# Kernel tuning notes

Hardware: AMD Instinct MI355X
Metric: run time of the kernel (lower is better)

Reference implementation:

```python
import jax, jax.numpy as jnp
import numpy as np

B, N, H, DH, E, D_IN = 2, 2048, 8, 32, 65536, 256
O = H * DH
SCALE = float(np.sqrt(DH))


def setup_inputs() -> dict:
    key = jax.random.key(0)
    ks = jax.random.split(key, 8)
    rng = np.random.default_rng(0)
    x = jax.random.normal(ks[0], (B, N, D_IN), jnp.float32)
    adj = jax.random.uniform(ks[1], (B, N, N), jnp.float32)
    # unique edges per graph so scatter-add matches torch advanced-index +=
    flat = np.stack([rng.choice(N * N, size=E, replace=False) for _ in range(B)])
    edge_index = jnp.asarray(np.stack([flat // N, flat % N], axis=1), jnp.int32)  # [B,2,E]
    edge_attr = jax.random.normal(ks[2], (B, E, H), jnp.float32)
    mask = jnp.ones((B, N), dtype=bool)
    qkv_w = jax.random.normal(ks[3], (D_IN, 3 * O), jnp.float32) / np.sqrt(D_IN)
    qkv_b = jnp.zeros((3 * O,), jnp.float32)
    e_w1 = jax.random.normal(ks[4], (H, H), jnp.float32) / np.sqrt(H)
    e_b1 = jnp.zeros((H,), jnp.float32)
    e_w2 = jax.random.normal(ks[5], (H, H), jnp.float32) / np.sqrt(H)
    e_b2 = jnp.zeros((H,), jnp.float32)
    shifts = jnp.asarray(np.linspace(0.1, 0.8, H), jnp.float32).reshape(1, H, 1, 1)
    widths = jnp.full((1, H, 1, 1), 0.5, jnp.float32)
    self_loop_W = jnp.asarray(1.0 / DH + rng.uniform(0, 1, H), jnp.float32).reshape(1, H, 1, 1)
    return dict(x=x, adj=adj, edge_attr=edge_attr, qkv_w=qkv_w, qkv_b=qkv_b,
                e_w1=e_w1, e_b1=e_b1, e_w2=e_w2, e_b2=e_b2,
                shifts=shifts, widths=widths, self_loop_W=self_loop_W,
                edge_index=edge_index, mask=mask)


def reference(x, adj, edge_attr, qkv_w, qkv_b, e_w1, e_b1, e_w2, e_b2,
              shifts, widths, self_loop_W, edge_index, mask):
    Bq, Nq = x.shape[0], x.shape[1]
    # qkv projection -> [3,B,H,N,DH]
    qkv = (x @ qkv_w + qkv_b).reshape(Bq, Nq, 3, H, DH)
    qkv = jnp.transpose(qkv, (2, 0, 3, 1, 4))
    Q, K, V = qkv[0], qkv[1], qkv[2]
    # edge FFN applied twice (eval mode: noise/dropout are identity)
    def ffn(e):
        return jax.nn.relu(e @ e_w1 + e_b1) @ e_w2 + e_b2
    ea = ffn(ffn(edge_attr))                      # [B,E,H]
    ea = jnp.transpose(ea, (0, 2, 1))             # [B,H,E]
    # scores + learned moire adjacency bias
    scores = jnp.einsum('bhqd,bhkd->bhqk', Q, K) / SCALE
    moire = jnp.exp(-((adj[:, None] - shifts) ** 2) / (2.0 * widths ** 2))  # gaussian focus
    moire = jnp.clip(moire, 1e-6, None)
    s = scores + jnp.log(moire)                   # [B,H,N,N]
    # scatter edge features into score matrix
    u = edge_index[:, 0, :]                        # [B,E]
    v = edge_index[:, 1, :]
    bi = jnp.arange(Bq)[:, None, None]
    hi = jnp.arange(H)[None, :, None]
    s = s.at[bi, hi, u[:, None, :], v[:, None, :]].add(ea)
    # self-loop diagonal bias (non-trainable)
    s = s + jnp.eye(Nq, dtype=s.dtype)[None, None] * self_loop_W
    # mask and softmax
    m2 = mask[:, None, :] & mask[:, :, None]       # [B,N,N]
    s = jnp.where(m2[:, None], s, jnp.asarray(-1e6, s.dtype))
    attn = jax.nn.softmax(s, axis=-1)
    out = jnp.einsum('bhqk,bhkd->bhqd', attn, V)
    return jnp.transpose(out, (0, 2, 1, 3)).reshape(Bq, Nq, O)
```

## Files before the change

### kernel.cpp

```cpp
#include <hip/hip_runtime.h>

#define B_ 2
#define N_ 2048
#define H_ 8
#define DH_ 32
#define E_ 65536
#define DIN_ 256
#define KT 256
#define ECAP 32
#define QSCALE 0.2550348872f
#define LOG2E 1.4426950408889634f
#define LOG2MIN -19.931568569324174f

typedef short bf16x8 __attribute__((ext_vector_type(8)));
typedef float floatx4 __attribute__((ext_vector_type(4)));

__device__ __forceinline__ unsigned short f2b(float f){
  union { float f; unsigned int u; } v; v.f = f;
  return (unsigned short)((v.u + 0x7fffu + ((v.u >> 16) & 1u)) >> 16);
}
__device__ __forceinline__ bf16x8 f8_to_bf(const float* p){
  float4 a = *(const float4*)p, b = *(const float4*)(p + 4);
  bf16x8 r;
  r[0] = (short)f2b(a.x); r[1] = (short)f2b(a.y); r[2] = (short)f2b(a.z); r[3] = (short)f2b(a.w);
  r[4] = (short)f2b(b.x); r[5] = (short)f2b(b.y); r[6] = (short)f2b(b.z); r[7] = (short)f2b(b.w);
  return r;
}
__device__ __forceinline__ unsigned int cvt_pk_bf16(float lo, float hi){
  unsigned int r;
  asm("v_cvt_pk_bf16_f32 %0, %1, %2" : "=v"(r) : "v"(lo), "v"(hi));
  return r;
}

__global__ __launch_bounds__(256) void prep_kernel(
    const float* __restrict__ eattr,
    const float* __restrict__ w1, const float* __restrict__ b1,
    const float* __restrict__ w2, const float* __restrict__ b2,
    float* __restrict__ ea,
    const int* __restrict__ ei, int* __restrict__ cnt, unsigned int* __restrict__ pck,
    const float* __restrict__ w, unsigned short* __restrict__ wT)
{
  int bb = blockIdx.x, tid = threadIdx.x;
  if (bb < 512){
    __shared__ float W1[64], W2[64], Bv1[8], Bv2[8];
    if (tid < 64){ W1[tid] = w1[tid]; W2[tid] = w2[tid]; }
    if (tid < 8){ Bv1[tid] = b1[tid]; Bv2[tid] = b2[tid]; }
    __syncthreads();
    int gid = bb * 256 + tid;
    const float* ep = eattr + (size_t)gid * 8;
    float cur[8];
#pragma unroll
    for (int i = 0; i < 8; ++i) cur[i] = ep[i];
#pragma unroll
    for (int pass = 0; pass < 2; ++pass){
      float t[8];
#pragma unroll
      for (int j = 0; j < 8; ++j){
        float s = Bv1[j];
#pragma unroll
        for (int i = 0; i < 8; ++i) s += cur[i] * W1[i * 8 + j];
        t[j] = fmaxf(s, 0.f);
      }
#pragma unroll
      for (int j = 0; j < 8; ++j){
        float s = Bv2[j];
#pragma unroll
        for (int i = 0; i < 8; ++i) s += t[i] * W2[i * 8 + j];
        cur[j] = s;
      }
    }
    float* op = ea + (size_t)gid * 8;
#pragma unroll
    for (int j = 0; j < 8; ++j) op[j] = cur[j] * LOG2E;
  } else if (bb < 1024){
    int gid = (bb - 512) * 256 + tid;
    int b = gid >> 16, e = gid & (E_ - 1);
    int u = ei[(size_t)b * 2 * E_ + e];
    int v = ei[(size_t)b * 2 * E_ + E_ + e];
    int bucket = ((b << 11) + u) * 8 + (v >> 8);
    int slot = atomicAdd(&cnt[bucket], 1);
    if (slot < ECAP) pck[(size_t)bucket * ECAP + slot] = ((unsigned int)e << 11) | (unsigned int)v;
  } else {
    int k = bb - 1024;
    for (int c = tid; c < 768; c += 256)
      wT[(size_t)c * 256 + k] = f2b(w[(size_t)k * 768 + c]);
  }
}

__global__ __launch_bounds__(256) void qkv_kernel(
    const float* __restrict__ x, const unsigned short* __restrict__ wT,
    const float* __restrict__ bias,
    unsigned short* __restrict__ Qb, unsigned short* __restrict__ Kb, unsigned short* __restrict__ Vt)
{
  int tid = threadIdx.x;
  int wave = tid >> 6, lane = tid & 63, m = lane & 15, quad = lane >> 4;
  int rowbase = blockIdx.x * 16;
  int colbase = blockIdx.y * 64 + wave * 16;
  floatx4 acc = {0.f, 0.f, 0.f, 0.f};
#pragma unroll
  for (int kb = 0; kb < 8; ++kb){
    bf16x8 af = f8_to_bf(x + (size_t)(rowbase + m) * DIN_ + kb * 32 + quad * 8);
    bf16x8 bf = *(const bf16x8*)(wT + (size_t)(colbase + m) * DIN_ + kb * 32 + quad * 8);
    acc = __builtin_amdgcn_mfma_f32_16x16x32_bf16(af, bf, acc, 0, 0, 0);
  }
  int ccol = colbase + m;
  int which = ccol >> 8, hh = (ccol >> 5) & 7, dh = ccol & 31;
  float bv = bias[ccol];
  int row0 = rowbase + quad * 4;
  int bidx = row0 >> 11, n0 = row0 & (N_ - 1);
  size_t bh = (size_t)(bidx * H_ + hh);
  if (which == 0){
#pragma unroll
    for (int r = 0; r < 4; ++r)
      Qb[(bh * N_ + n0 + r) * DH_ + dh] = f2b((acc[r] + bv) * QSCALE);
  } else if (which == 1){
#pragma unroll
    for (int r = 0; r < 4; ++r)
      Kb[(bh * N_ + n0 + r) * DH_ + dh] = f2b(acc[r] + bv);
  } else {
    ushort4 st;
    st.x = f2b(acc[0] + bv); st.y = f2b(acc[1] + bv);
    st.z = f2b(acc[2] + bv); st.w = f2b(acc[3] + bv);
    *(ushort4*)(Vt + (bh * DH_ + dh) * N_ + n0) = st;
  }
}

__global__ __launch_bounds__(256) void attn_kernel(
    const unsigned short* __restrict__ Qb, const unsigned short* __restrict__ Kb,
    const unsigned short* __restrict__ Vt, const float* __restrict__ adj,
    const float* __restrict__ ea, const int* __restrict__ cnt, const unsigned int* __restrict__ pck,
    const float* __restrict__ shifts, const float* __restrict__ widths,
    const float* __restrict__ selfW, float* __restrict__ out)
{
  __shared__ float S[4][16][68];
  __shared__ float mfin[4][16], lfin[4][16];

  int bid = blockIdx.x;
  int qt = bid & 127, h = (bid >> 7) & 7, b = bid >> 10;
  int qbase = qt * 16;
  int tid = threadIdx.x, wave = tid >> 6, lane = tid & 63, m = lane & 15, quad = lane >> 4;
  float shift_h = shifts[h];
  float w_h = widths[h];
  float i2w_h = LOG2E / (2.f * w_h * w_h);
  float selfW_h = selfW[h] * LOG2E;
  size_t krow = (size_t)(b * H_ + h) * N_;
  size_t vrow = (size_t)(b * H_ + h) * DH_;
  bf16x8 qfrag = *(const bf16x8*)(Qb + (krow + qbase + m) * DH_ + quad * 8);
  float (*Sw)[68] = S[wave];

  int rr = lane >> 2, sl0 = lane & 3;
  const int* cntp = cnt + ((size_t)(b * N_) + qbase + rr) * 8;
  const unsigned int* pckp = pck + ((size_t)((b * N_ + qbase + rr) * 8)) * ECAP;
  const float* eabase = ea + (size_t)b * E_ * H_ + h;
  const float* adjp = adj + ((size_t)b * N_ + qbase + m) * N_ + wave * 64 + quad * 8;
  const unsigned short* vp0 = Vt + (vrow + m) * N_ + wave * 64 + quad * 8;
  const unsigned short* vp1 = Vt + (vrow + 16 + m) * N_ + wave * 64 + quad * 8;
  const unsigned short* kp  = Kb + (krow + wave * 64 + m) * DH_ + quad * 8;

  float mcur = -1e30f, lcur = 0.f;
  floatx4 oacc0 = {0.f, 0.f, 0.f, 0.f};
  floatx4 oacc1 = {0.f, 0.f, 0.f, 0.f};

  for (int kt = 0; kt < N_ / KT; ++kt){
    int k0 = kt * KT;
    int dq = qbase - k0 - wave * 64;
#pragma unroll
    for (int s = 0; s < 4; ++s){
      bf16x8 kf = *(const bf16x8*)(kp + (size_t)(k0 + s * 16) * DH_);
      floatx4 acc = {0.f, 0.f, 0.f, 0.f};
      acc = __builtin_amdgcn_mfma_f32_16x16x32_bf16(qfrag, kf, acc, 0, 0, 0);
      int t = s * 16 + m - dq;
#pragma unroll
      for (int r = 0; r < 4; ++r){
        float v = acc[r];
        if (t == quad * 4 + r) v += selfW_h;
        Sw[quad * 4 + r][s * 16 + m] = v;
      }
    }
    asm volatile("s_waitcnt lgkmcnt(0)" ::: "memory");
    {
      int nb = cntp[kt]; nb = nb > ECAP ? ECAP : nb;
      const unsigned int* pb = pckp + kt * ECAP;
      for (int slot = sl0; slot < nb; slot += 4){
        unsigned int pk = pb[slot];
        int vv = (int)(pk & (unsigned int)(N_ - 1));
        int c = vv - k0 - wave * 64;
        if ((unsigned)c < 64u){
          int e = (int)(pk >> 11);
          Sw[rr][c] += eabase[(size_t)e * H_];
        }
      }
    }
    asm volatile("s_waitcnt lgkmcnt(0)" ::: "memory");
    const float* sp = &Sw[m][quad * 8];
    float4 s00 = *(const float4*)(sp);
    float4 s01 = *(const float4*)(sp + 4);
    float4 s10 = *(const float4*)(sp + 32);
    float4 s11 = *(const float4*)(sp + 36);
    const float* ap = adjp + k0;
    float4 a00 = *(const float4*)(ap);
    float4 a01 = *(const float4*)(ap + 4);
    float4 a10 = *(const float4*)(ap + 32);
    float4 a11 = *(const float4*)(ap + 36);
    bf16x8 vf00 = *(const bf16x8*)(vp0 + k0);
    bf16x8 vf01 = *(const bf16x8*)(vp1 + k0);
    bf16x8 vf10 = *(const bf16x8*)(vp0 + k0 + 32);
    bf16x8 vf11 = *(const bf16x8*)(vp1 + k0 + 32);
    float dd;
    dd = a00.x - shift_h; s00.x += fmaxf(-dd * dd * i2w_h, LOG2MIN);
    dd = a00.y - shift_h; s00.y += fmaxf(-dd * dd * i2w_h, LOG2MIN);
    dd = a00.z - shift_h; s00.z += fmaxf(-dd * dd * i2w_h, LOG2MIN);
    dd = a00.w - shift_h; s00.w += fmaxf(-dd * dd * i2w_h, LOG2MIN);
    dd = a01.x - shift_h; s01.x += fmaxf(-dd * dd * i2w_h, LOG2MIN);
    dd = a01.y - shift_h; s01.y += fmaxf(-dd * dd * i2w_h, LOG2MIN);
    dd = a01.z - shift_h; s01.z += fmaxf(-dd * dd * i2w_h, LOG2MIN);
    dd = a01.w - shift_h; s01.w += fmaxf(-dd * dd * i2w_h, LOG2MIN);
    dd = a10.x - shift_h; s10.x += fmaxf(-dd * dd * i2w_h, LOG2MIN);
    dd = a10.y - shift_h; s10.y += fmaxf(-dd * dd * i2w_h, LOG2MIN);
    dd = a10.z - shift_h; s10.z += fmaxf(-dd * dd * i2w_h, LOG2MIN);
    dd = a10.w - shift_h; s10.w += fmaxf(-dd * dd * i2w_h, LOG2MIN);
    dd = a11.x - shift_h; s11.x += fmaxf(-dd * dd * i2w_h, LOG2MIN);
    dd = a11.y - shift_h; s11.y += fmaxf(-dd * dd * i2w_h, LOG2MIN);
    dd = a11.z - shift_h; s11.z += fmaxf(-dd * dd * i2w_h, LOG2MIN);
    dd = a11.w - shift_h; s11.w += fmaxf(-dd * dd * i2w_h, LOG2MIN);
    float lm = fmaxf(fmaxf(fmaxf(s00.x, s00.y), fmaxf(s00.z, s00.w)),
                     fmaxf(fmaxf(s01.x, s01.y), fmaxf(s01.z, s01.w)));
    lm = fmaxf(lm, fmaxf(fmaxf(fmaxf(s10.x, s10.y), fmaxf(s10.z, s10.w)),
                         fmaxf(fmaxf(s11.x, s11.y), fmaxf(s11.z, s11.w))));
    lm = fmaxf(lm, __shfl_xor(lm, 16));
    lm = fmaxf(lm, __shfl_xor(lm, 32));
    float mnew = fmaxf(mcur, lm);
    float al = exp2f(mcur - mnew);
    mcur = mnew;
    float al0 = __shfl(al, quad * 4 + 0);
    float al1 = __shfl(al, quad * 4 + 1);
    float al2 = __shfl(al, quad * 4 + 2);
    float al3 = __shfl(al, quad * 4 + 3);
    oacc0[0] *= al0; oacc0[1] *= al1; oacc0[2] *= al2; oacc0[3] *= al3;
    oacc1[0] *= al0; oacc1[1] *= al1; oacc1[2] *= al2; oacc1[3] *= al3;
    float ps = 0.f, p0, p1;
    union { bf16x8 v; unsigned int u[4]; } P;
    p0 = exp2f(s00.x - mcur); p1 = exp2f(s00.y - mcur); ps += p0 + p1; P.u[0] = cvt_pk_bf16(p0, p1);
    p0 = exp2f(s00.z - mcur); p1 = exp2f(s00.w - mcur); ps += p0 + p1; P.u[1] = cvt_pk_bf16(p0, p1);
    p0 = exp2f(s01.x - mcur); p1 = exp2f(s01.y - mcur); ps += p0 + p1; P.u[2] = cvt_pk_bf16(p0, p1);
    p0 = exp2f(s01.z - mcur); p1 = exp2f(s01.w - mcur); ps += p0 + p1; P.u[3] = cvt_pk_bf16(p0, p1);
    oacc0 = __builtin_amdgcn_mfma_f32_16x16x32_bf16(P.v, vf00, oacc0, 0, 0, 0);
    oacc1 = __builtin_amdgcn_mfma_f32_16x16x32_bf16(P.v, vf01, oacc1, 0, 0, 0);
    p0 = exp2f(s10.x - mcur); p1 = exp2f(s10.y - mcur); ps += p0 + p1; P.u[0] = cvt_pk_bf16(p0, p1);
    p0 = exp2f(s10.z - mcur); p1 = exp2f(s10.w - mcur); ps += p0 + p1; P.u[1] = cvt_pk_bf16(p0, p1);
    p0 = exp2f(s11.x - mcur); p1 = exp2f(s11.y - mcur); ps += p0 + p1; P.u[2] = cvt_pk_bf16(p0, p1);
    p0 = exp2f(s11.z - mcur); p1 = exp2f(s11.w - mcur); ps += p0 + p1; P.u[3] = cvt_pk_bf16(p0, p1);
    oacc0 = __builtin_amdgcn_mfma_f32_16x16x32_bf16(P.v, vf10, oacc0, 0, 0, 0);
    oacc1 = __builtin_amdgcn_mfma_f32_16x16x32_bf16(P.v, vf11, oacc1, 0, 0, 0);
    ps += __shfl_xor(ps, 16);
    ps += __shfl_xor(ps, 32);
    lcur = lcur * al + ps;
  }

  if (quad == 0){ mfin[wave][m] = mcur; lfin[wave][m] = lcur; }
  float* Ow = &S[wave][0][0];
#pragma unroll
  for (int r = 0; r < 4; ++r){
    Ow[(quad * 4 + r) * 32 + m]      = oacc0[r];
    Ow[(quad * 4 + r) * 32 + 16 + m] = oacc1[r];
  }
  __syncthreads();
  const float* Sv = &S[0][0][0];
#pragma unroll
  for (int ii = 0; ii < 2; ++ii){
    int i = tid + ii * 256;
    int r = i >> 5, dcol = i & 31;
    float m0 = mfin[0][r], m1 = mfin[1][r], m2 = mfin[2][r], m3 = mfin[3][r];
    float mg = fmaxf(fmaxf(m0, m1), fmaxf(m2, m3));
    float w0 = exp2f(m0 - mg), w1 = exp2f(m1 - mg);
    float w2 = exp2f(m2 - mg), w3 = exp2f(m3 - mg);
    int o_idx = r * 32 + dcol;
    float o = Sv[o_idx] * w0 + Sv[1088 + o_idx] * w1
            + Sv[2176 + o_idx] * w2 + Sv[3264 + o_idx] * w3;
    float l = lfin[0][r] * w0 + lfin[1][r] * w1 + lfin[2][r] * w2 + lfin[3][r] * w3;
    out[((size_t)b * N_ + qbase + r) * (H_ * DH_) + h * DH_ + dcol] = o / l;
  }
}

extern "C" void kernel_launch(void* const* d_in, const int* in_sizes, int n_in,
                              void* d_out, int out_size, void* d_ws, size_t ws_size,
                              hipStream_t stream)
{
  const float* x      = (const float*)d_in[0];
  const float* adj    = (const float*)d_in[1];
  const float* eattr  = (const float*)d_in[2];
  const float* qkvw   = (const float*)d_in[3];
  const float* qkvb   = (const float*)d_in[4];
  const float* ew1    = (const float*)d_in[5];
  const float* eb1    = (const float*)d_in[6];
  const float* ew2    = (const float*)d_in[7];
  const float* eb2    = (const float*)d_in[8];
  const float* shifts = (const float*)d_in[9];
  const float* widths = (const float*)d_in[10];
  const float* selfW  = (const float*)d_in[11];
  const int*   ei     = (const int*)d_in[12];
  float* out = (float*)d_out;

  char* ws = (char*)d_ws;
  unsigned short* Qb  = (unsigned short*)(ws);
  unsigned short* Kb  = (unsigned short*)(ws + ((size_t)2 << 20));
  unsigned short* Vt  = (unsigned short*)(ws + ((size_t)4 << 20));
  unsigned short* wT  = (unsigned short*)(ws + ((size_t)6 << 20));
  float*          ea  = (float*)(ws + ((size_t)7 << 20));
  int*            cnt = (int*)(ws + ((size_t)11 << 20));
  unsigned int*  pck  = (unsigned int*)(ws + ((size_t)12 << 20));

  hipMemsetAsync(cnt, 0, (size_t)B_ * N_ * 8 * sizeof(int), stream);
  hipLaunchKernelGGL(prep_kernel, dim3(1280), dim3(256), 0, stream,
                     eattr, ew1, eb1, ew2, eb2, ea, ei, cnt, pck, qkvw, wT);
  hipLaunchKernelGGL(qkv_kernel, dim3(256, 12), dim3(256), 0, stream, x, wT, qkvb, Qb, Kb, Vt);
  hipLaunchKernelGGL(attn_kernel, dim3(B_ * H_ * (N_ / 16)), dim3(256), 0, stream,
                     Qb, Kb, Vt, adj, ea, cnt, pck, shifts, widths, selfW, out);
}
```

Before: 234.3 us.

## Prefetch next tile's edge entries, use raw v_exp, simplify diagonal bias

The attention loop now loads the next key tile's edge count, its first two packed edges per lane and their edge-feature values while the current tile computes. This hides the serial global-load latency of the edge scatter. It also hoists the adjacency loads earlier, fully unrolls the tile loop and applies the self-loop bias with a single diagonal write instead of a per-element compare. exp2f is replaced with the raw v_exp_f32 instruction and the Gaussian bias is vectorised. The cost is higher register pressure, and the raw exp drops denormal handling.

```diff
diff --git a/kernel.cpp b/kernel.cpp
--- a/kernel.cpp
+++ b/kernel.cpp
@@ -7,6 +7,7 @@
 #define E_ 65536
 #define DIN_ 256
 #define KT 256
+#define NKT (N_ / KT)
 #define ECAP 32
 #define QSCALE 0.2550348872f
 #define LOG2E 1.4426950408889634f
@@ -29,6 +30,11 @@
 __device__ __forceinline__ unsigned int cvt_pk_bf16(float lo, float hi){
   unsigned int r;
   asm("v_cvt_pk_bf16_f32 %0, %1, %2" : "=v"(r) : "v"(lo), "v"(hi));
+  return r;
+}
+__device__ __forceinline__ float fexp2(float x){
+  float r;
+  asm("v_exp_f32 %0, %1" : "=v"(r) : "v"(x));
   return r;
 }
 
@@ -147,82 +153,101 @@
   size_t vrow = (size_t)(b * H_ + h) * DH_;
   bf16x8 qfrag = *(const bf16x8*)(Qb + (krow + qbase + m) * DH_ + quad * 8);
   float (*Sw)[68] = S[wave];
+  int wcol = wave * 64;
 
   int rr = lane >> 2, sl0 = lane & 3;
   const int* cntp = cnt + ((size_t)(b * N_) + qbase + rr) * 8;
   const unsigned int* pckp = pck + ((size_t)((b * N_ + qbase + rr) * 8)) * ECAP;
   const float* eabase = ea + (size_t)b * E_ * H_ + h;
-  const float* adjp = adj + ((size_t)b * N_ + qbase + m) * N_ + wave * 64 + quad * 8;
-  const unsigned short* vp0 = Vt + (vrow + m) * N_ + wave * 64 + quad * 8;
-  const unsigned short* vp1 = Vt + (vrow + 16 + m) * N_ + wave * 64 + quad * 8;
-  const unsigned short* kp  = Kb + (krow + wave * 64 + m) * DH_ + quad * 8;
+  const float* adjp = adj + ((size_t)b * N_ + qbase + m) * N_ + wcol + quad * 8;
+  const unsigned short* vp0 = Vt + (vrow + m) * N_ + wcol + quad * 8;
+  const unsigned short* vp1 = Vt + (vrow + 16 + m) * N_ + wcol + quad * 8;
+  const unsigned short* kp  = Kb + (krow + wcol + m) * DH_ + quad * 8;
+
+  floatx4 sh4 = {shift_h, shift_h, shift_h, shift_h};
+  floatx4 ni4 = {-i2w_h, -i2w_h, -i2w_h, -i2w_h};
+  floatx4 lm4 = {LOG2MIN, LOG2MIN, LOG2MIN, LOG2MIN};
 
   float mcur = -1e30f, lcur = 0.f;
   floatx4 oacc0 = {0.f, 0.f, 0.f, 0.f};
   floatx4 oacc1 = {0.f, 0.f, 0.f, 0.f};
 
-  for (int kt = 0; kt < N_ / KT; ++kt){
+  int nb_c = cntp[0]; nb_c = nb_c > ECAP ? ECAP : nb_c;
+  unsigned int pk0 = pckp[sl0];
+  unsigned int pk1 = pckp[sl0 + 4];
+  int c0_c = (int)(pk0 & (N_ - 1)) - wcol;
+  int c1_c = (int)(pk1 & (N_ - 1)) - wcol;
+  bool g0_c = (sl0 < nb_c) && ((unsigned)c0_c < 64u);
+  bool g1_c = (sl0 + 4 < nb_c) && ((unsigned)c1_c < 64u);
+  float ea0_c = 0.f, ea1_c = 0.f;
+  if (g0_c) ea0_c = eabase[(size_t)(pk0 >> 11) * H_];
+  if (g1_c) ea1_c = eabase[(size_t)(pk1 >> 11) * H_];
+
+#pragma unroll
+  for (int kt = 0; kt < NKT; ++kt){
     int k0 = kt * KT;
-    int dq = qbase - k0 - wave * 64;
+    int nb_n = 0; unsigned int pk0_n = 0, pk1_n = 0;
+    if (kt + 1 < NKT){
+      nb_n  = cntp[kt + 1];
+      pk0_n = pckp[(kt + 1) * ECAP + sl0];
+      pk1_n = pckp[(kt + 1) * ECAP + sl0 + 4];
+    }
+    const float* ap = adjp + k0;
+    floatx4 a00 = *(const floatx4*)(ap);
+    floatx4 a01 = *(const floatx4*)(ap + 4);
+    floatx4 a10 = *(const floatx4*)(ap + 32);
+    floatx4 a11 = *(const floatx4*)(ap + 36);
+
 #pragma unroll
     for (int s = 0; s < 4; ++s){
       bf16x8 kf = *(const bf16x8*)(kp + (size_t)(k0 + s * 16) * DH_);
       floatx4 acc = {0.f, 0.f, 0.f, 0.f};
       acc = __builtin_amdgcn_mfma_f32_16x16x32_bf16(qfrag, kf, acc, 0, 0, 0);
-      int t = s * 16 + m - dq;
-#pragma unroll
-      for (int r = 0; r < 4; ++r){
-        float v = acc[r];
-        if (t == quad * 4 + r) v += selfW_h;
-        Sw[quad * 4 + r][s * 16 + m] = v;
+#pragma unroll
+      for (int r = 0; r < 4; ++r)
+        Sw[quad * 4 + r][s * 16 + m] = acc[r];
+    }
+    {
+      int dw = qbase - k0 - wcol;
+      if ((unsigned)dw < 64u && lane < 16)
+        Sw[lane][dw + lane] += selfW_h;
+    }
+    if (g0_c) Sw[rr][c0_c] += ea0_c;
+    if (g1_c) Sw[rr][c1_c] += ea1_c;
+    if (nb_c > 8){
+      for (int slot = sl0 + 8; slot < nb_c; slot += 4){
+        unsigned int p = pckp[kt * ECAP + slot];
+        int vv = (int)(p & (N_ - 1));
+        int c = vv - k0 - wcol;
+        if ((unsigned)c < 64u) Sw[rr][c] += eabase[(size_t)(p >> 11) * H_];
       }
     }
-    asm volatile("s_waitcnt lgkmcnt(0)" ::: "memory");
-    {
-      int nb = cntp[kt]; nb = nb > ECAP ? ECAP : nb;
-      const unsigned int* pb = pckp + kt * ECAP;
-      for (int slot = sl0; slot < nb; slot += 4){
-        unsigned int pk = pb[slot];
-        int vv = (int)(pk & (unsigned int)(N_ - 1));
-        int c = vv - k0 - wave * 64;
-        if ((unsigned)c < 64u){
-          int e = (int)(pk >> 11);
-          Sw[rr][c] += eabase[(size_t)e * H_];
-        }
-      }
-    }
-    asm volatile("s_waitcnt lgkmcnt(0)" ::: "memory");
-    const float* sp = &Sw[m][quad * 8];
-    float4 s00 = *(const float4*)(sp);
-    float4 s01 = *(const float4*)(sp + 4);
-    float4 s10 = *(const float4*)(sp + 32);
-    float4 s11 = *(const float4*)(sp + 36);
-    const float* ap = adjp + k0;
-    float4 a00 = *(const float4*)(ap);
-    float4 a01 = *(const float4*)(ap + 4);
-    float4 a10 = *(const float4*)(ap + 32);
-    float4 a11 = *(const float4*)(ap + 36);
+    int c0_n = 0, c1_n = 0; bool g0_n = false, g1_n = false;
+    float ea0_n = 0.f, ea1_n = 0.f;
+    if (kt + 1 < NKT){
+      nb_n = nb_n > ECAP ? ECAP : nb_n;
+      c0_n = (int)(pk0_n & (N_ - 1)) - (k0 + KT) - wcol;
+      c1_n = (int)(pk1_n & (N_ - 1)) - (k0 + KT) - wcol;
+      g0_n = (sl0 < nb_n) && ((unsigned)c0_n < 64u);
+      g1_n = (sl0 + 4 < nb_n) && ((unsigned)c1_n < 64u);
+      if (g0_n) ea0_n = eabase[(size_t)(pk0_n >> 11) * H_];
+      if (g1_n) ea1_n = eabase[(size_t)(pk1_n >> 11) * H_];
+    }
     bf16x8 vf00 = *(const bf16x8*)(vp0 + k0);
     bf16x8 vf01 = *(const bf16x8*)(vp1 + k0);
     bf16x8 vf10 = *(const bf16x8*)(vp0 + k0 + 32);
     bf16x8 vf11 = *(const bf16x8*)(vp1 + k0 + 32);
-    float dd;
-    dd = a00.x - shift_h; s00.x += fmaxf(-dd * dd * i2w_h, LOG2MIN);
-    dd = a00.y - shift_h; s00.y += fmaxf(-dd * dd * i2w_h, LOG2MIN);
-    dd = a00.z - shift_h; s00.z += fmaxf(-dd * dd * i2w_h, LOG2MIN);
-    dd = a00.w - shift_h; s00.w += fmaxf(-dd * dd * i2w_h, LOG2MIN);
-    dd = a01.x - shift_h; s01.x += fmaxf(-dd * dd * i2w_h, LOG2MIN);
-    dd = a01.y - shift_h; s01.y += fmaxf(-dd * dd * i2w_h, LOG2MIN);
-    dd = a01.z - shift_h; s01.z += fmaxf(-dd * dd * i2w_h, LOG2MIN);
-    dd = a01.w - shift_h; s01.w += fmaxf(-dd * dd * i2w_h, LOG2MIN);
-    dd = a10.x - shift_h; s10.x += fmaxf(-dd * dd * i2w_h, LOG2MIN);
-    dd = a10.y - shift_h; s10.y += fmaxf(-dd * dd * i2w_h, LOG2MIN);
-    dd = a10.z - shift_h; s10.z += fmaxf(-dd * dd * i2w_h, LOG2MIN);
-    dd = a10.w - shift_h; s10.w += fmaxf(-dd * dd * i2w_h, LOG2MIN);
-    dd = a11.x - shift_h; s11.x += fmaxf(-dd * dd * i2w_h, LOG2MIN);
-    dd = a11.y - shift_h; s11.y += fmaxf(-dd * dd * i2w_h, LOG2MIN);
-    dd = a11.z - shift_h; s11.z += fmaxf(-dd * dd * i2w_h, LOG2MIN);
-    dd = a11.w - shift_h; s11.w += fmaxf(-dd * dd * i2w_h, LOG2MIN);
+
+    const float* sp = &Sw[m][quad * 8];
+    floatx4 s00 = *(const floatx4*)(sp);
+    floatx4 s01 = *(const floatx4*)(sp + 4);
+    floatx4 s10 = *(const floatx4*)(sp + 32);
+    floatx4 s11 = *(const floatx4*)(sp + 36);
+    floatx4 d;
+    d = a00 - sh4; s00 += __builtin_elementwise_max(d * d * ni4, lm4);
+    d = a01 - sh4; s01 += __builtin_elementwise_max(d * d * ni4, lm4);
+    d = a10 - sh4; s10 += __builtin_elementwise_max(d * d * ni4, lm4);
+    d = a11 - sh4; s11 += __builtin_elementwise_max(d * d * ni4, lm4);
     float lm = fmaxf(fmaxf(fmaxf(s00.x, s00.y), fmaxf(s00.z, s00.w)),
                      fmaxf(fmaxf(s01.x, s01.y), fmaxf(s01.z, s01.w)));
     lm = fmaxf(lm, fmaxf(fmaxf(fmaxf(s10.x, s10.y), fmaxf(s10.z, s10.w)),
@@ -230,7 +255,7 @@
     lm = fmaxf(lm, __shfl_xor(lm, 16));
     lm = fmaxf(lm, __shfl_xor(lm, 32));
     float mnew = fmaxf(mcur, lm);
-    float al = exp2f(mcur - mnew);
+    float al = fexp2(mcur - mnew);
     mcur = mnew;
     float al0 = __shfl(al, quad * 4 + 0);
     float al1 = __shfl(al, quad * 4 + 1);
@@ -238,23 +263,27 @@
     float al3 = __shfl(al, quad * 4 + 3);
     oacc0[0] *= al0; oacc0[1] *= al1; oacc0[2] *= al2; oacc0[3] *= al3;
     oacc1[0] *= al0; oacc1[1] *= al1; oacc1[2] *= al2; oacc1[3] *= al3;
+    floatx4 m4 = {mcur, mcur, mcur, mcur};
+    floatx4 e0v = s00 - m4, e1v = s01 - m4, e2v = s10 - m4, e3v = s11 - m4;
     float ps = 0.f, p0, p1;
     union { bf16x8 v; unsigned int u[4]; } P;
-    p0 = exp2f(s00.x - mcur); p1 = exp2f(s00.y - mcur); ps += p0 + p1; P.u[0] = cvt_pk_bf16(p0, p1);
-    p0 = exp2f(s00.z - mcur); p1 = exp2f(s00.w - mcur); ps += p0 + p1; P.u[1] = cvt_pk_bf16(p0, p1);
-    p0 = exp2f(s01.x - mcur); p1 = exp2f(s01.y - mcur); ps += p0 + p1; P.u[2] = cvt_pk_bf16(p0, p1);
-    p0 = exp2f(s01.z - mcur); p1 = exp2f(s01.w - mcur); ps += p0 + p1; P.u[3] = cvt_pk_bf16(p0, p1);
+    p0 = fexp2(e0v.x); p1 = fexp2(e0v.y); ps += p0 + p1; P.u[0] = cvt_pk_bf16(p0, p1);
+    p0 = fexp2(e0v.z); p1 = fexp2(e0v.w); ps += p0 + p1; P.u[1] = cvt_pk_bf16(p0, p1);
+    p0 = fexp2(e1v.x); p1 = fexp2(e1v.y); ps += p0 + p1; P.u[2] = cvt_pk_bf16(p0, p1);
+    p0 = fexp2(e1v.z); p1 = fexp2(e1v.w); ps += p0 + p1; P.u[3] = cvt_pk_bf16(p0, p1);
     oacc0 = __builtin_amdgcn_mfma_f32_16x16x32_bf16(P.v, vf00, oacc0, 0, 0, 0);
     oacc1 = __builtin_amdgcn_mfma_f32_16x16x32_bf16(P.v, vf01, oacc1, 0, 0, 0);
-    p0 = exp2f(s10.x - mcur); p1 = exp2f(s10.y - mcur); ps += p0 + p1; P.u[0] = cvt_pk_bf16(p0, p1);
-    p0 = exp2f(s10.z - mcur); p1 = exp2f(s10.w - mcur); ps += p0 + p1; P.u[1] = cvt_pk_bf16(p0, p1);
-    p0 = exp2f(s11.x - mcur); p1 = exp2f(s11.y - mcur); ps += p0 + p1; P.u[2] = cvt_pk_bf16(p0, p1);
-    p0 = exp2f(s11.z - mcur); p1 = exp2f(s11.w - mcur); ps += p0 + p1; P.u[3] = cvt_pk_bf16(p0, p1);
+    p0 = fexp2(e2v.x); p1 = fexp2(e2v.y); ps += p0 + p1; P.u[0] = cvt_pk_bf16(p0, p1);
+    p0 = fexp2(e2v.z); p1 = fexp2(e2v.w); ps += p0 + p1; P.u[1] = cvt_pk_bf16(p0, p1);
+    p0 = fexp2(e3v.x); p1 = fexp2(e3v.y); ps += p0 + p1; P.u[2] = cvt_pk_bf16(p0, p1);
+    p0 = fexp2(e3v.z); p1 = fexp2(e3v.w); ps += p0 + p1; P.u[3] = cvt_pk_bf16(p0, p1);
     oacc0 = __builtin_amdgcn_mfma_f32_16x16x32_bf16(P.v, vf10, oacc0, 0, 0, 0);
     oacc1 = __builtin_amdgcn_mfma_f32_16x16x32_bf16(P.v, vf11, oacc1, 0, 0, 0);
     ps += __shfl_xor(ps, 16);
     ps += __shfl_xor(ps, 32);
     lcur = lcur * al + ps;
+    nb_c = nb_n; g0_c = g0_n; g1_c = g1_n;
+    c0_c = c0_n; c1_c = c1_n; ea0_c = ea0_n; ea1_c = ea1_n;
   }
 
   if (quad == 0){ mfin[wave][m] = mcur; lfin[wave][m] = lcur; }
@@ -272,8 +301,8 @@
     int r = i >> 5, dcol = i & 31;
     float m0 = mfin[0][r], m1 = mfin[1][r], m2 = mfin[2][r], m3 = mfin[3][r];
     float mg = fmaxf(fmaxf(m0, m1), fmaxf(m2, m3));
-    float w0 = exp2f(m0 - mg), w1 = exp2f(m1 - mg);
-    float w2 = exp2f(m2 - mg), w3 = exp2f(m3 - mg);
+    float w0 = fexp2(m0 - mg), w1 = fexp2(m1 - mg);
+    float w2 = fexp2(m2 - mg), w3 = fexp2(m3 - mg);
     int o_idx = r * 32 + dcol;
     float o = Sv[o_idx] * w0 + Sv[1088 + o_idx] * w1
             + Sv[2176 + o_idx] * w2 + Sv[3264 + o_idx] * w3;
```

Result: no change. 235.0 us (+0.3%).
